# Kernel optimization log

Hardware: AMD Instinct MI355X
Metric: run time of the kernel (lower is better)

The kernel has to match this reference:

```python
import jax, jax.numpy as jnp
import numpy as np
from jax import lax

EPS = 1e-5

def _zpool(x):
    # cat(max over channel, mean over channel) -> [B,2,H,W]
    return jnp.concatenate([x.max(axis=1, keepdims=True), x.mean(axis=1, keepdims=True)], axis=1)

def _gate(x, w, g, b, m, v):
    # ZPool -> 7x7 conv (2->1, same pad) -> inference BN -> sigmoid -> scale input
    z = _zpool(x)
    y = lax.conv_general_dilated(z, w, (1, 1), [(3, 3), (3, 3)],
                                 dimension_numbers=('NCHW', 'OIHW', 'NCHW'))
    scale = g / jnp.sqrt(v + EPS)
    y = (y - m[None, :, None, None]) * scale[None, :, None, None] + b[None, :, None, None]
    return x * jax.nn.sigmoid(y)


def setup_inputs() -> dict:
    key = jax.random.key(0)
    ks = jax.random.split(key, 8)
    B, C, H, W = 8, 256, 64, 64
    inp = {
        'x': jax.random.normal(ks[0], (B, C, H, W), dtype=jnp.float32),
        'w_cw': jax.random.normal(ks[1], (1, 2, 7, 7), dtype=jnp.float32) * 0.1,
        'g_cw': jnp.ones((1,), jnp.float32), 'b_cw': jnp.zeros((1,), jnp.float32),
        'm_cw': jnp.zeros((1,), jnp.float32), 'v_cw': jnp.ones((1,), jnp.float32),
        'w_hc': jax.random.normal(ks[2], (1, 2, 7, 7), dtype=jnp.float32) * 0.1,
        'g_hc': jnp.ones((1,), jnp.float32), 'b_hc': jnp.zeros((1,), jnp.float32),
        'm_hc': jnp.zeros((1,), jnp.float32), 'v_hc': jnp.ones((1,), jnp.float32),
        'w_hw': jax.random.normal(ks[3], (1, 2, 7, 7), dtype=jnp.float32) * 0.1,
        'g_hw': jnp.ones((1,), jnp.float32), 'b_hw': jnp.zeros((1,), jnp.float32),
        'm_hw': jnp.zeros((1,), jnp.float32), 'v_hw': jnp.ones((1,), jnp.float32),
        'w1d': jax.random.normal(ks[4], (3, 1, 7), dtype=jnp.float32) * 0.1,
    }
    return inp


def reference(x, w_cw, g_cw, b_cw, m_cw, v_cw,
              w_hc, g_hc, b_hc, m_hc, v_hc,
              w_hw, g_hw, b_hw, m_hw, v_hw, w1d):
    # branch 1: attend over (C) with H as channel dim
    b1 = _gate(x.transpose(0, 2, 1, 3), w_cw, g_cw, b_cw, m_cw, v_cw).transpose(0, 2, 1, 3)
    # branch 2: attend with W as channel dim
    b2 = _gate(x.transpose(0, 3, 2, 1), w_hc, g_hc, b_hc, m_hc, v_hc).transpose(0, 3, 2, 1)
    # branch 3: spatial attention in native layout
    b3 = _gate(x, w_hw, g_hw, b_hw, m_hw, v_hw)

    x_out = (b1 + b2 + b3) / 3.0
    pooled = x_out.mean(axis=(2, 3))                     # [B, C]
    logits = lax.conv_general_dilated(pooled[:, None, :], w1d, (1,), [(3, 3)],
                                      dimension_numbers=('NCH', 'OIH', 'NCH'))  # [B,3,C]
    wts = jax.nn.softmax(logits, axis=1)[..., None, None]  # [B,3,C,1,1]
    branches = jnp.stack([b1, b2, b3], axis=1)             # [B,3,C,H,W]
    return (wts * branches).sum(axis=1)
```

## Files before the change

### kernel.cpp

```cpp
#include <hip/hip_runtime.h>
#include <math.h>

#define BB 8
#define CC 256
#define HH 64
#define WW 64
#define EPS 1e-5f
#define PSCALE (1.f / 12288.f)

__global__ __launch_bounds__(256) void pool_kernel(
    const float* __restrict__ x,
    float* __restrict__ z1max, float* __restrict__ z1mean,
    float* __restrict__ z2tmax, float* __restrict__ z2tmean,
    float* __restrict__ z3max, float* __restrict__ z3mean,
    float* __restrict__ pooled)
{
    __shared__ float smem[HH * 65 + 512];
    int blk = blockIdx.x;
    int t = threadIdx.x;

    if (blk < 8) pooled[blk * 256 + t] = 0.f;

    if (blk < BB * CC) {
        int bc = blk;
        const float4* xt4 = (const float4*)x + (size_t)bc * 1024;
        float* tile = smem;
        float* red  = smem + HH * 65;

        #pragma unroll
        for (int i = 0; i < 4; ++i) {
            int idx = t + i * 256;
            float4 v = xt4[idx];
            int h = idx >> 4, w0 = (idx & 15) * 4;
            float* d = &tile[h * 65 + w0];
            d[0] = v.x; d[1] = v.y; d[2] = v.z; d[3] = v.w;
        }
        __syncthreads();

        {
            int w = t & 63, hg = t >> 6;
            float m = -INFINITY, s = 0.f;
            #pragma unroll
            for (int i = 0; i < 16; ++i) {
                float v = tile[(hg * 16 + i) * 65 + w];
                m = fmaxf(m, v); s += v;
            }
            red[t] = m; red[256 + t] = s;
        }
        __syncthreads();
        if (t < 64) {
            float m = red[t], s = red[256 + t];
            #pragma unroll
            for (int g = 1; g < 4; ++g) { m = fmaxf(m, red[g * 64 + t]); s += red[256 + g * 64 + t]; }
            z1max [bc * WW + t] = m;
            z1mean[bc * WW + t] = s * (1.f / 64.f);
        }
        __syncthreads();

        {
            int h = t & 63, wg = t >> 6;
            float m = -INFINITY, s = 0.f;
            #pragma unroll
            for (int i = 0; i < 16; ++i) {
                float v = tile[h * 65 + wg * 16 + i];
                m = fmaxf(m, v); s += v;
            }
            red[t] = m; red[256 + t] = s;
        }
        __syncthreads();
        if (t < 64) {
            float m = red[t], s = red[256 + t];
            #pragma unroll
            for (int g = 1; g < 4; ++g) { m = fmaxf(m, red[g * 64 + t]); s += red[256 + g * 64 + t]; }
            z2tmax [bc * HH + t] = m;
            z2tmean[bc * HH + t] = s * (1.f / 64.f);
        }
    } else {
        int bh = blk - BB * CC;
        int b = bh >> 6, h = bh & 63;
        int wq = t & 15, cgp = t >> 4;

        const float4* base = (const float4*)x
            + ((size_t)b * CC * HH * WW + (size_t)h * WW) / 4 + wq;
        float4 m = make_float4(-INFINITY, -INFINITY, -INFINITY, -INFINITY);
        float4 s = make_float4(0.f, 0.f, 0.f, 0.f);
        #pragma unroll 4
        for (int i = 0; i < 16; ++i) {
            float4 v = base[(size_t)(cgp * 16 + i) * 1024];
            m.x = fmaxf(m.x, v.x); m.y = fmaxf(m.y, v.y);
            m.z = fmaxf(m.z, v.z); m.w = fmaxf(m.w, v.w);
            s.x += v.x; s.y += v.y; s.z += v.z; s.w += v.w;
        }
        float4* mred = (float4*)smem;
        float4* sred = (float4*)smem + 256;
        mred[t] = m; sred[t] = s;
        __syncthreads();
        if (t < 16) {
            float4 mm = mred[t], ss = sred[t];
            #pragma unroll
            for (int g = 1; g < 16; ++g) {
                float4 mv = mred[g * 16 + t], sv = sred[g * 16 + t];
                mm.x = fmaxf(mm.x, mv.x); mm.y = fmaxf(mm.y, mv.y);
                mm.z = fmaxf(mm.z, mv.z); mm.w = fmaxf(mm.w, mv.w);
                ss.x += sv.x; ss.y += sv.y; ss.z += sv.z; ss.w += sv.w;
            }
            ss.x *= (1.f / 256.f); ss.y *= (1.f / 256.f);
            ss.z *= (1.f / 256.f); ss.w *= (1.f / 256.f);
            *(float4*)(z3max  + bh * WW + t * 4) = mm;
            *(float4*)(z3mean + bh * WW + t * 4) = ss;
        }
    }
}

template<int TR>
__device__ __forceinline__ float conv_gate(
    const float* __restrict__ zm, const float* __restrict__ za,
    const float* __restrict__ wp, const float* gp, const float* bp,
    const float* mp, const float* vp,
    int R, int Cw, int b, int r, int col)
{
    const float* zmb = zm + (size_t)b * R * Cw;
    const float* zab = za + (size_t)b * R * Cw;
    float acc = 0.f;
    #pragma unroll
    for (int dr = 0; dr < 7; ++dr) {
        int rr = r + dr - 3;
        if (rr < 0 || rr >= R) continue;
        #pragma unroll
        for (int dc = 0; dc < 7; ++dc) {
            int cc2 = col + dc - 3;
            if (cc2 < 0 || cc2 >= Cw) continue;
            const int wi = TR ? (dc * 7 + dr) : (dr * 7 + dc);
            acc += wp[wi]      * zmb[rr * Cw + cc2]
                 + wp[49 + wi] * zab[rr * Cw + cc2];
        }
    }
    float scale = gp[0] * rsqrtf(vp[0] + EPS);
    float y = (acc - mp[0]) * scale + bp[0];
    return 1.f / (1.f + __expf(-y));
}

__global__ __launch_bounds__(256) void gate_kernel(
    const float* __restrict__ x,
    const float* __restrict__ z1max, const float* __restrict__ z1mean,
    const float* __restrict__ w0p, const float* g0, const float* b0,
    const float* m0, const float* v0, float* __restrict__ s1,
    const float* __restrict__ z2tmax, const float* __restrict__ z2tmean,
    const float* __restrict__ w1p, const float* g1, const float* b1,
    const float* m1, const float* v1, float* __restrict__ s2,
    const float* __restrict__ z3max, const float* __restrict__ z3mean,
    const float* __restrict__ w2p, const float* g2, const float* b2,
    const float* m2, const float* v2, float* __restrict__ s3,
    float* __restrict__ pooled)
{
    int blk = blockIdx.x;
    int t = threadIdx.x;

    if (blk < 512) {
        int o = blk * 256 + t;
        int b = o >> 14, rem = o & 16383;
        int r = rem >> 6, col = o & 63;
        float v = conv_gate<0>(z1max, z1mean, w0p, g0, b0, m0, v0, CC, WW, b, r, col);
        s1[o] = v;
        float prod = v * z1mean[o];
        #pragma unroll
        for (int off = 32; off >= 1; off >>= 1) prod += __shfl_down(prod, off);
        if ((t & 63) == 0) atomicAdd(&pooled[o >> 6], 64.f * prod);
    } else if (blk < 1024) {
        int o = (blk - 512) * 256 + t;
        int b = o >> 14, rem = o & 16383;
        int r = rem >> 6, col = o & 63;
        float v = conv_gate<1>(z2tmax, z2tmean, w1p, g1, b1, m1, v1, CC, HH, b, r, col);
        s2[o] = v;
        float prod = v * z2tmean[o];
        #pragma unroll
        for (int off = 32; off >= 1; off >>= 1) prod += __shfl_down(prod, off);
        if ((t & 63) == 0) atomicAdd(&pooled[o >> 6], 64.f * prod);
    } else {
        __shared__ float s3row[WW];
        int bh = blk - 1024;
        int b = bh >> 6, h = bh & 63;
        if (t < 64) {
            float v = conv_gate<0>(z3max, z3mean, w2p, g2, b2, m2, v2, HH, WW, b, h, t);
            s3[bh * WW + t] = v;
            s3row[t] = v;
        }
        __syncthreads();

        int wv = t >> 6, l = t & 63;
        int c_local = l >> 2, wsub = l & 3;
        const float4* s3q4 = (const float4*)s3row;

        #pragma unroll 1
        for (int pass = 0; pass < 4; ++pass) {
            int c = pass * 64 + (wv << 4) + c_local;
            const float4* xr4 = (const float4*)x
                + ((size_t)(b * 256 + c) * 4096 + h * 64) / 4 + wsub * 4;
            float acc = 0.f;
            #pragma unroll
            for (int j = 0; j < 4; ++j) {
                float4 xv = xr4[j];
                float4 sv = s3q4[wsub * 4 + j];
                acc += xv.x * sv.x + xv.y * sv.y + xv.z * sv.z + xv.w * sv.w;
            }
            acc += __shfl_xor(acc, 1);
            acc += __shfl_xor(acc, 2);
            if (wsub == 0) atomicAdd(&pooled[b * 256 + c], acc);
        }
    }
}

__global__ __launch_bounds__(256) void final_kernel(
    const float* __restrict__ x,
    const float* __restrict__ s1, const float* __restrict__ s2,
    const float* __restrict__ s3, const float* __restrict__ pooled,
    const float* __restrict__ w1d, float* __restrict__ out)
{
    __shared__ float kk[3];
    int t = threadIdx.x;
    int i4 = blockIdx.x * 256 + t;
    int rest = i4 >> 4;
    int h = rest & 63;
    int c = (rest >> 6) & 255;
    int b = rest >> 14;

    if (t == 0) {
        float lg0 = 0.f, lg1 = 0.f, lg2 = 0.f;
        #pragma unroll
        for (int jj = 0; jj < 7; ++jj) {
            int cc2 = c + jj - 3;
            float pv = (cc2 >= 0 && cc2 < CC) ? pooled[b * CC + cc2] : 0.f;
            lg0 += w1d[jj] * pv;
            lg1 += w1d[7 + jj] * pv;
            lg2 += w1d[14 + jj] * pv;
        }
        lg0 *= PSCALE; lg1 *= PSCALE; lg2 *= PSCALE;
        float mx = fmaxf(lg0, fmaxf(lg1, lg2));
        float e0 = __expf(lg0 - mx), e1 = __expf(lg1 - mx), e2 = __expf(lg2 - mx);
        float inv = 1.f / (e0 + e1 + e2);
        kk[0] = e0 * inv; kk[1] = e1 * inv; kk[2] = e2 * inv;
    }
    __syncthreads();
    float k0 = kk[0], k1 = kk[1], k2 = kk[2];

    int w0 = (i4 & 15) * 4;
    const float4 x4  = *(const float4*)(x  + (size_t)i4 * 4);
    const float4 s1v = *(const float4*)(s1 + ((size_t)(b * CC + c)) * WW + w0);
    const float  s2v = s2[rest];
    const float4 s3v = *(const float4*)(s3 + ((size_t)(b * HH + h)) * WW + w0);

    float4 o;
    o.x = x4.x * (k0 * s1v.x + k1 * s2v + k2 * s3v.x);
    o.y = x4.y * (k0 * s1v.y + k1 * s2v + k2 * s3v.y);
    o.z = x4.z * (k0 * s1v.z + k1 * s2v + k2 * s3v.z);
    o.w = x4.w * (k0 * s1v.w + k1 * s2v + k2 * s3v.w);
    *(float4*)(out + (size_t)i4 * 4) = o;
}

extern "C" void kernel_launch(void* const* d_in, const int* in_sizes, int n_in,
                              void* d_out, int out_size, void* d_ws, size_t ws_size,
                              hipStream_t stream)
{
    const float* x    = (const float*)d_in[0];
    const float* w_cw = (const float*)d_in[1];
    const float* g_cw = (const float*)d_in[2];
    const float* b_cw = (const float*)d_in[3];
    const float* m_cw = (const float*)d_in[4];
    const float* v_cw = (const float*)d_in[5];
    const float* w_hc = (const float*)d_in[6];
    const float* g_hc = (const float*)d_in[7];
    const float* b_hc = (const float*)d_in[8];
    const float* m_hc = (const float*)d_in[9];
    const float* v_hc = (const float*)d_in[10];
    const float* w_hw = (const float*)d_in[11];
    const float* g_hw = (const float*)d_in[12];
    const float* b_hw = (const float*)d_in[13];
    const float* m_hw = (const float*)d_in[14];
    const float* v_hw = (const float*)d_in[15];
    const float* w1d  = (const float*)d_in[16];
    float* out = (float*)d_out;

    float* ws = (float*)d_ws;
    const size_t N1 = (size_t)BB * CC * WW;
    const size_t N2 = (size_t)BB * CC * HH;
    const size_t N3 = (size_t)BB * HH * WW;
    float* z1max   = ws;
    float* z1mean  = z1max   + N1;
    float* z2tmax  = z1mean  + N1;
    float* z2tmean = z2tmax  + N2;
    float* z3max   = z2tmean + N2;
    float* z3mean  = z3max   + N3;
    float* s1      = z3mean  + N3;
    float* s2      = s1 + N1;
    float* s3      = s2 + N2;
    float* pooled  = s3 + N3;

    pool_kernel<<<BB * CC + BB * HH, 256, 0, stream>>>(
        x, z1max, z1mean, z2tmax, z2tmean, z3max, z3mean, pooled);

    gate_kernel<<<1536, 256, 0, stream>>>(
        x,
        z1max, z1mean, w_cw, g_cw, b_cw, m_cw, v_cw, s1,
        z2tmax, z2tmean, w_hc, g_hc, b_hc, m_hc, v_hc, s2,
        z3max, z3mean, w_hw, g_hw, b_hw, m_hw, v_hw, s3,
        pooled);

    final_kernel<<<(BB * CC * HH * WW / 4) / 256, 256, 0, stream>>>(
        x, s1, s2, s3, pooled, w1d, out);
}
```

Baseline: 141.7 us.

## Tile gate 7x7 convs through shared memory with register output blocking

Branches 1 and 2 of the gate kernel now stage a 38x70 padded tile of the pooled max/mean maps and the weights in shared memory. Each thread computes 8 output rows from register accumulators, replacing the earlier scheme of one output per thread read straight from global memory. The grid drops from 1024 to 128 blocks for those branches. Branch 3 also stages its 7-row halo in shared memory and issues all 16 x float4 loads before reducing, to get more memory-level parallelism. The risks are lower parallelism with only 128 tile blocks and higher register use.

```diff
diff --git a/kernel.cpp b/kernel.cpp
--- a/kernel.cpp
+++ b/kernel.cpp
@@ -112,33 +112,9 @@
     }
 }
 
-template<int TR>
-__device__ __forceinline__ float conv_gate(
-    const float* __restrict__ zm, const float* __restrict__ za,
-    const float* __restrict__ wp, const float* gp, const float* bp,
-    const float* mp, const float* vp,
-    int R, int Cw, int b, int r, int col)
-{
-    const float* zmb = zm + (size_t)b * R * Cw;
-    const float* zab = za + (size_t)b * R * Cw;
-    float acc = 0.f;
-    #pragma unroll
-    for (int dr = 0; dr < 7; ++dr) {
-        int rr = r + dr - 3;
-        if (rr < 0 || rr >= R) continue;
-        #pragma unroll
-        for (int dc = 0; dc < 7; ++dc) {
-            int cc2 = col + dc - 3;
-            if (cc2 < 0 || cc2 >= Cw) continue;
-            const int wi = TR ? (dc * 7 + dr) : (dr * 7 + dc);
-            acc += wp[wi]      * zmb[rr * Cw + cc2]
-                 + wp[49 + wi] * zab[rr * Cw + cc2];
-        }
-    }
-    float scale = gp[0] * rsqrtf(vp[0] + EPS);
-    float y = (acc - mp[0]) * scale + bp[0];
-    return 1.f / (1.f + __expf(-y));
-}
+#define TROWS 38
+#define TPITCH 70
+#define TELEMS (TROWS * TPITCH)
 
 __global__ __launch_bounds__(256) void gate_kernel(
     const float* __restrict__ x,
@@ -153,35 +129,114 @@
     const float* m2, const float* v2, float* __restrict__ s3,
     float* __restrict__ pooled)
 {
+    __shared__ float sm[2 * TELEMS + 100];
     int blk = blockIdx.x;
     int t = threadIdx.x;
 
-    if (blk < 512) {
-        int o = blk * 256 + t;
-        int b = o >> 14, rem = o & 16383;
-        int r = rem >> 6, col = o & 63;
-        float v = conv_gate<0>(z1max, z1mean, w0p, g0, b0, m0, v0, CC, WW, b, r, col);
-        s1[o] = v;
-        float prod = v * z1mean[o];
-        #pragma unroll
-        for (int off = 32; off >= 1; off >>= 1) prod += __shfl_down(prod, off);
-        if ((t & 63) == 0) atomicAdd(&pooled[o >> 6], 64.f * prod);
-    } else if (blk < 1024) {
-        int o = (blk - 512) * 256 + t;
-        int b = o >> 14, rem = o & 16383;
-        int r = rem >> 6, col = o & 63;
-        float v = conv_gate<1>(z2tmax, z2tmean, w1p, g1, b1, m1, v1, CC, HH, b, r, col);
-        s2[o] = v;
-        float prod = v * z2tmean[o];
-        #pragma unroll
-        for (int off = 32; off >= 1; off >>= 1) prod += __shfl_down(prod, off);
-        if ((t & 63) == 0) atomicAdd(&pooled[o >> 6], 64.f * prod);
+    if (blk < 128) {
+        const int br  = blk >> 6;
+        const int sub = blk & 63;
+        const int b   = sub >> 3;
+        const int rt  = (sub & 7) * 32;
+        const float* zm = br ? z2tmax  : z1max;
+        const float* za = br ? z2tmean : z1mean;
+        const float* wp = br ? w1p : w0p;
+        const float* gp = br ? g1 : g0;  const float* bp = br ? b1 : b0;
+        const float* mp = br ? m1 : m0;  const float* vp = br ? v1 : v0;
+        float* sout = br ? s2 : s1;
+
+        float* tm  = sm;
+        float* ta  = sm + TELEMS;
+        float* wsm = sm + 2 * TELEMS;
+
+        if (t < 98) {
+            int p = (t >= 49) ? 1 : 0;
+            int q = t - p * 49;
+            wsm[t] = wp[p * 49 + (br ? (q % 7) * 7 + q / 7 : q)];
+        }
+        for (int idx = t; idx < TELEMS; idx += 256) {
+            int r  = idx / TPITCH;
+            int cc = idx - r * TPITCH;
+            int grow = rt + r - 3, gcol = cc - 3;
+            bool ok = (grow >= 0) & (grow < 256) & (gcol >= 0) & (gcol < 64);
+            size_t gi = ((size_t)b * 256 + grow) * 64 + gcol;
+            tm[idx] = ok ? zm[gi] : 0.f;
+            ta[idx] = ok ? za[gi] : 0.f;
+        }
+        __syncthreads();
+
+        const int col = t & 63, rg = t >> 6;
+        const int lo0 = rg * 8;
+
+        float acc[8];
+        #pragma unroll
+        for (int o = 0; o < 8; ++o) acc[o] = 0.f;
+
+        #pragma unroll
+        for (int rl = 0; rl < 14; ++rl) {
+            const float* rowm = &tm[(lo0 + rl) * TPITCH + col];
+            const float* rowa = &ta[(lo0 + rl) * TPITCH + col];
+            #pragma unroll
+            for (int dc = 0; dc < 7; ++dc) {
+                float vmax = rowm[dc], vmean = rowa[dc];
+                #pragma unroll
+                for (int o = 0; o < 8; ++o) {
+                    int dr = rl - o;
+                    if (dr >= 0 && dr < 7) {
+                        acc[o] = fmaf(wsm[dr * 7 + dc],      vmax,  acc[o]);
+                        acc[o] = fmaf(wsm[49 + dr * 7 + dc], vmean, acc[o]);
+                    }
+                }
+            }
+        }
+
+        const float bnscale = gp[0] * rsqrtf(vp[0] + EPS);
+        const float bnmean = mp[0], bnbias = bp[0];
+        #pragma unroll
+        for (int o = 0; o < 8; ++o) {
+            int lo = lo0 + o;
+            float y = (acc[o] - bnmean) * bnscale + bnbias;
+            float sv = 1.f / (1.f + __expf(-y));
+            sout[((size_t)b * 256 + rt + lo) * 64 + col] = sv;
+            float prod = sv * ta[(lo + 3) * TPITCH + col + 3];
+            #pragma unroll
+            for (int off = 32; off >= 1; off >>= 1) prod += __shfl_down(prod, off);
+            if ((t & 63) == 0) atomicAdd(&pooled[b * 256 + rt + lo], 64.f * prod);
+        }
     } else {
-        __shared__ float s3row[WW];
-        int bh = blk - 1024;
+        float* t3m   = sm;
+        float* t3a   = sm + 7 * TPITCH;
+        float* w2sm  = sm + 14 * TPITCH;
+        float* s3row = sm + 14 * TPITCH + 98;
+
+        int bh = blk - 128;
         int b = bh >> 6, h = bh & 63;
+
+        if (t < 98) w2sm[t] = w2p[t];
+        for (int idx = t; idx < 7 * TPITCH; idx += 256) {
+            int r  = idx / TPITCH;
+            int cc = idx - r * TPITCH;
+            int grow = h + r - 3, gcol = cc - 3;
+            bool ok = (grow >= 0) & (grow < 64) & (gcol >= 0) & (gcol < 64);
+            size_t gi = ((size_t)b * 64 + grow) * 64 + gcol;
+            t3m[idx] = ok ? z3max[gi]  : 0.f;
+            t3a[idx] = ok ? z3mean[gi] : 0.f;
+        }
+        __syncthreads();
+
         if (t < 64) {
-            float v = conv_gate<0>(z3max, z3mean, w2p, g2, b2, m2, v2, HH, WW, b, h, t);
+            float acc = 0.f;
+            #pragma unroll
+            for (int dr = 0; dr < 7; ++dr) {
+                #pragma unroll
+                for (int dc = 0; dc < 7; ++dc) {
+                    acc = fmaf(w2sm[dr * 7 + dc],      t3m[dr * TPITCH + t + dc], acc);
+                    acc = fmaf(w2sm[49 + dr * 7 + dc], t3a[dr * TPITCH + t + dc], acc);
+                }
+            }
+            float scale = g2[0] * rsqrtf(v2[0] + EPS);
+            float y = (acc - m2[0]) * scale + b2[0];
+            float v = 1.f / (1.f + __expf(-y));
             s3[bh * WW + t] = v;
             s3row[t] = v;
         }
@@ -191,17 +246,24 @@
         int c_local = l >> 2, wsub = l & 3;
         const float4* s3q4 = (const float4*)s3row;
 
-        #pragma unroll 1
+        float4 xv[16];
+        #pragma unroll
         for (int pass = 0; pass < 4; ++pass) {
             int c = pass * 64 + (wv << 4) + c_local;
             const float4* xr4 = (const float4*)x
                 + ((size_t)(b * 256 + c) * 4096 + h * 64) / 4 + wsub * 4;
+            #pragma unroll
+            for (int j = 0; j < 4; ++j) xv[pass * 4 + j] = xr4[j];
+        }
+        #pragma unroll
+        for (int pass = 0; pass < 4; ++pass) {
+            int c = pass * 64 + (wv << 4) + c_local;
             float acc = 0.f;
             #pragma unroll
             for (int j = 0; j < 4; ++j) {
-                float4 xv = xr4[j];
+                float4 a = xv[pass * 4 + j];
                 float4 sv = s3q4[wsub * 4 + j];
-                acc += xv.x * sv.x + xv.y * sv.y + xv.z * sv.z + xv.w * sv.w;
+                acc += a.x * sv.x + a.y * sv.y + a.z * sv.z + a.w * sv.w;
             }
             acc += __shfl_xor(acc, 1);
             acc += __shfl_xor(acc, 2);
@@ -298,7 +360,7 @@
     pool_kernel<<<BB * CC + BB * HH, 256, 0, stream>>>(
         x, z1max, z1mean, z2tmax, z2tmean, z3max, z3mean, pooled);
 
-    gate_kernel<<<1536, 256, 0, stream>>>(
+    gate_kernel<<<128 + BB * HH, 256, 0, stream>>>(
         x,
         z1max, z1mean, w_cw, g_cw, b_cw, m_cw, v_cw, s1,
         z2tmax, z2tmean, w_hc, g_hc, b_hc, m_hc, v_hc, s2,
```

Result: no change. 141.9 us, median of 2 (+0.1%).
